# Kernel tuning notes

Hardware: AMD Instinct MI355X
Metric: run time of the kernel (lower is better)

## Reference

```python
import jax, jax.numpy as jnp
import numpy as np

N_CLASSES = 300
EMPTY = N_CLASSES
ALPHA, GAMMA = 0.25, 2.0
W_CLS, W_DOA, W_LOUD, W_CONF, W_SCE = 1.0, 1.0, 0.5, 1.0, 0.3
L_CLS, L_DOA, L_CONF = 1.0, 1.0, 0.5  # matching cost weights


def _lsa(cost):
    """Rectangular linear sum assignment (Jonker-Volgenant / e-maxx Hungarian).
    Returns (row_idx, col_idx) matching min(P,G) pairs, same optimum as scipy."""
    transposed = cost.shape[0] > cost.shape[1]
    C = cost.T if transposed else cost
    n, m = C.shape  # n <= m
    INF = float('inf')
    u = [0.0] * (n + 1)
    v = [0.0] * (m + 1)
    p = [0] * (m + 1)
    for i in range(1, n + 1):
        p[0] = i
        j0 = 0
        minv = [INF] * (m + 1)
        way = [0] * (m + 1)
        used = [False] * (m + 1)
        while True:
            used[j0] = True
            i0 = p[j0]
            delta = INF
            j1 = 0
            for j in range(1, m + 1):
                if not used[j]:
                    cur = C[i0 - 1, j - 1] - u[i0] - v[j]
                    if cur < minv[j]:
                        minv[j] = cur
                        way[j] = j0
                    if minv[j] < delta:
                        delta = minv[j]
                        j1 = j
            for j in range(m + 1):
                if used[j]:
                    u[p[j]] += delta
                    v[j] -= delta
                else:
                    minv[j] -= delta
            j0 = j1
            if p[j0] == 0:
                break
        while j0:
            j1 = way[j0]
            p[j0] = p[j1]
            j0 = j1
    rows, cols = [], []
    for j in range(1, m + 1):
        if p[j]:
            rows.append(p[j] - 1)
            cols.append(j - 1)
    r = np.asarray(rows, np.int64)
    c = np.asarray(cols, np.int64)
    if transposed:
        r, c = c, r
    return r, c


def _match(cl, dv, conf, gcls, gdoa, gmask):
    """Per-frame Hungarian matching (no-grad, host numpy), faithful to hungarian_match.
    Returns matched mask (B,T,S) bool, per-slot target class (B,T,S) int32 (EMPTY if unmatched),
    and gather index into gt slots (B,T,S) int32 (0 where unmatched; masked out later)."""
    B, T, S, C = cl.shape
    z = cl - cl.max(-1, keepdims=True)
    prob = np.exp(z)
    prob /= prob.sum(-1, keepdims=True)
    prob = prob[..., :N_CLASSES]
    dn = dv / np.maximum(np.linalg.norm(dv, axis=-1, keepdims=True), 1e-12)
    cp = 1.0 / (1.0 + np.exp(-conf))
    matched = np.zeros((B, T, S), bool)
    tgt = np.full((B, T, S), EMPTY, np.int32)
    gidx = np.zeros((B, T, S), np.int32)
    for b in range(B):
        for t in range(T):
            act = np.nonzero(gmask[b, t])[0]
            if act.size == 0:
                continue
            gc = gcls[b, t, act]
            gd = gdoa[b, t, act]
            gdn = gd / np.maximum(np.linalg.norm(gd, axis=-1, keepdims=True), 1e-12)
            cost = (L_CLS * (-prob[b, t][:, gc])
                    + L_DOA * (1.0 - dn[b, t] @ gdn.T)
                    + L_CONF * (1.0 - cp[b, t])[:, None])
            r, c = _lsa(cost.astype(np.float64))
            matched[b, t, r] = True
            tgt[b, t, r] = gc[c]
            gidx[b, t, r] = act[c]
    return matched, tgt, gidx


def _loss(class_logits, doa_vec, loudness, confidence, sce_vec, gt_doa, gt_loud,
          matched, tgt_cls, gidx):
    B, T, S, _ = class_logits.shape
    dt = class_logits.dtype
    mf = matched.astype(dt)                      # (B,T,S)
    # focal loss (target = matched gt class, else EMPTY)
    logp = jax.nn.log_softmax(class_logits, axis=-1)
    ce = -jnp.take_along_axis(logp, tgt_cls[..., None].astype(jnp.int32), axis=-1)[..., 0]
    f = ALPHA * (1.0 - jnp.exp(-ce)) ** GAMMA * ce
    Gm = mf.sum(-1)                              # (B,T) matched count
    Um = S - Gm
    safeG = jnp.maximum(Gm, 1.0)
    safeU = jnp.maximum(Um, 1.0)
    cls_fr = (jnp.where(Gm > 0, (f * mf).sum(-1) / safeG, 0.0)
              + jnp.where(Um > 0, (f * (1.0 - mf)).sum(-1) / safeU, 0.0))
    # gather matched gt doa / loud per slot
    g3 = jnp.broadcast_to(gidx[..., None].astype(jnp.int32), gt_doa.shape)
    mdoa = jnp.take_along_axis(gt_doa, g3, axis=2)       # (B,T,S,3)
    mloud = jnp.take_along_axis(gt_loud, gidx.astype(jnp.int32), axis=2)
    # DOA cosine distance (torch cosine_similarity eps=1e-8)
    eps = 1e-8
    num = (doa_vec * mdoa).sum(-1)
    den = (jnp.maximum(jnp.linalg.norm(doa_vec, axis=-1), eps)
           * jnp.maximum(jnp.linalg.norm(mdoa, axis=-1), eps))
    d = 1.0 - num / den
    doa_fr = jnp.where(Gm > 0, (d * mf).sum(-1) / safeG, 0.0)
    # smooth L1 (beta=1)
    diff = loudness - mloud
    ad = jnp.abs(diff)
    sl1 = jnp.where(ad < 1.0, 0.5 * diff * diff, ad - 0.5)
    loud_fr = jnp.where(Gm > 0, (sl1 * mf).sum(-1) / safeG, 0.0)
    # BCE-with-logits, target = matched indicator (zeros if no gt)
    bce = jax.nn.softplus(confidence) - confidence * mf
    conf_fr = bce.mean(-1)
    # SCE: mse(sce, gt_doa * exp(gt_loud/20)) over matched slots
    gt_sce = mdoa * jnp.exp(mloud / 20.0)[..., None]
    sq = ((sce_vec - gt_sce) ** 2).mean(-1)
    sce_fr = jnp.where(Gm > 0, (sq * mf).sum(-1) / safeG, 0.0)
    norm = float(B * T)
    cls_l = W_CLS * cls_fr.sum() / norm
    doa_l = W_DOA * doa_fr.sum() / norm
    loud_l = W_LOUD * loud_fr.sum() / norm
    conf_l = W_CONF * conf_fr.sum() / norm
    sce_l = W_SCE * sce_fr.sum() / norm
    total = cls_l + doa_l + loud_l + conf_l + sce_l
    return jnp.stack([cls_l, doa_l, loud_l, conf_l, sce_l, total])


def setup_inputs() -> dict:
    key = jax.random.key(0)
    ks = jax.random.split(key, 9)
    B, T, S = 32, 256, 8
    C = N_CLASSES + 1
    return {
        "class_logits": jax.random.normal(ks[0], (B, T, S, C), jnp.float32),
        "doa_vec": jax.random.normal(ks[1], (B, T, S, 3), jnp.float32),
        "loudness": jax.random.normal(ks[2], (B, T, S), jnp.float32),
        "confidence": jax.random.normal(ks[3], (B, T, S), jnp.float32),
        "sce_vec": jax.random.normal(ks[4], (B, T, S, 3), jnp.float32),
        "gt_cls": jax.random.randint(ks[5], (B, T, S), 0, N_CLASSES, jnp.int32),
        "gt_doa": jax.random.normal(ks[6], (B, T, S, 3), jnp.float32),
        "gt_loud": jax.random.normal(ks[7], (B, T, S), jnp.float32),
        "gt_mask": jax.random.bernoulli(ks[8], 0.5, (B, T, S)),
    }


def reference(class_logits, doa_vec, loudness, confidence, sce_vec,
              gt_cls, gt_doa, gt_loud, gt_mask):
    matched, tgt, gidx = _match(np.asarray(class_logits), np.asarray(doa_vec),
                                np.asarray(confidence), np.asarray(gt_cls),
                                np.asarray(gt_doa), np.asarray(gt_mask))
    return _loss(class_logits, doa_vec, loudness, confidence, sce_vec,
                 gt_doa, gt_loud,
                 jnp.asarray(matched), jnp.asarray(tgt), jnp.asarray(gidx))
```

## Files before the change

### kernel.cpp

```cpp
#include <hip/hip_runtime.h>
#include <math.h>

#define NFRAMES 8192
#define NS 8
#define NC 301
#define NBLOCKS (NFRAMES / 4)

#define GLOBAL_AS __attribute__((address_space(1)))
#define LDS_AS    __attribute__((address_space(3)))

__device__ float g_partial[5 * NFRAMES];

__device__ __forceinline__ float readlanef(float x, int l) {
    return __int_as_float(__builtin_amdgcn_readlane(__float_as_int(x), l));
}

#define SWZ_F(x, OFF) __int_as_float(__builtin_amdgcn_ds_swizzle(__float_as_int(x), (OFF)))
#define SWZ_I(x, OFF) __builtin_amdgcn_ds_swizzle((x), (OFF))
#define OFF_X4  0x101F
#define OFF_X16 0x401F

#define DPP_F(x, CTRL) __int_as_float(__builtin_amdgcn_update_dpp(0, __float_as_int(x), (CTRL), 0xF, 0xF, true))
#define DPP_I(x, CTRL) __builtin_amdgcn_update_dpp(0, (x), (CTRL), 0xF, 0xF, true)
#define CTRL_X1 0xB1
#define CTRL_X2 0x4E
#define CTRL_X8 0x128

__global__ __launch_bounds__(256) void frame_kernel(
    const float* __restrict__ logits,
    const float* __restrict__ doa,
    const float* __restrict__ loud,
    const float* __restrict__ conf,
    const float* __restrict__ sce,
    const int*   __restrict__ gcls,
    const float* __restrict__ gdoa,
    const float* __restrict__ gloud,
    const unsigned int* __restrict__ gmaskw)
{
    __shared__ float lgs[4][NS * NC];

    const int lane = threadIdx.x & 63;
    const int wv   = threadIdx.x >> 6;
    const int f    = blockIdx.x * 4 + wv;
    const int s    = lane >> 3;
    const int g    = lane & 7;

    {
        const float4* src = reinterpret_cast<const float4*>(logits + (size_t)f * (NS * NC));
        char* dstb = reinterpret_cast<char*>(&lgs[wv][0]);
#pragma unroll
        for (int k = 0; k < 9; k++) {
            __builtin_amdgcn_global_load_lds(
                (const GLOBAL_AS void*)(src + (k << 6) + lane),
                (LDS_AS void*)(dstb + (k << 10)), 16, 0, 0);
        }
        if (lane < 602 - 576) {
            __builtin_amdgcn_global_load_lds(
                (const GLOBAL_AS void*)(src + 576 + lane),
                (LDS_AS void*)(dstb + 9 * 1024), 16, 0, 0);
        }
    }

    unsigned int mwd = gmaskw[lane];
    unsigned long long blo = __ballot((mwd & 0xFFFFFF00u) != 0);
    unsigned long long bf1 = __ballot(mwd == 0x3f800000u);
    const int mode = (blo == 0ull) ? 0 : (bf1 ? 2 : 1);

    float L_loud = 0.f, L_cf = 0.f, L_dx = 0.f, L_dy = 0.f, L_dz = 0.f;
    float L_s0 = 0.f, L_s1 = 0.f, L_s2 = 0.f;
    if (lane < 8) {
        size_t base = (size_t)f * NS + lane;
        L_loud = loud[base];  L_cf = conf[base];
        L_dx = doa[base * 3]; L_dy = doa[base * 3 + 1]; L_dz = doa[base * 3 + 2];
        L_s0 = sce[base * 3]; L_s1 = sce[base * 3 + 1]; L_s2 = sce[base * 3 + 2];
    }
    int gcv = (lane < 8) ? gcls[f * NS + lane] : 0;

    size_t sb3 = ((size_t)f * NS + s) * 3;
    float dxr = doa[sb3], dyr = doa[sb3 + 1], dzr = doa[sb3 + 2];
    float nn = fmaxf(sqrtf(dxr * dxr + dyr * dyr + dzr * dzr), 1e-12f);
    float dnx = dxr / nn, dny = dyr / nn, dnz = dzr / nn;
    float cp = 1.f / (1.f + __expf(-conf[(size_t)f * NS + s]));

    asm volatile("s_waitcnt vmcnt(0)" ::: "memory");

    const float* ls = &lgs[wv][s * NC];

    float z0 = 0.f, z1 = 0.f, z2 = 0.f, z3 = 0.f;
#pragma unroll
    for (int k = 0; k + 3 < 37; k += 4) {
        int c0 = g + (k << 3);
        z0 += __expf(ls[c0]);
        z1 += __expf(ls[c0 + 8]);
        z2 += __expf(ls[c0 + 16]);
        z3 += __expf(ls[c0 + 24]);
    }
    z0 += __expf(ls[g + (36 << 3)]);
    {
        int c = g + (37 << 3);
        if (c < NC) z1 += __expf(ls[c]);
    }
    float z = (z0 + z1) + (z2 + z3);
    z += DPP_F(z, CTRL_X1);
    z += DPP_F(z, CTRL_X2);
    z += SWZ_F(z, OFF_X4);
    const float A = __logf(z);
    const float lossA = __shfl(A, (lane & 7) << 3);

    int slotcls = __shfl(gcv, g);
    float myLgat = lgs[wv][s * NC + slotcls];
    float lossL300 = (lane < 8) ? lgs[wv][lane * NC + 300] : 0.f;

    bool on = false;
    if (lane < 8) {
        int idx = f * NS + lane;
        if (mode == 0)      on = ((const int*)gmaskw)[idx] != 0;
        else if (mode == 1) on = ((const unsigned char*)gmaskw)[idx] != 0;
        else                on = ((const float*)gmaskw)[idx] != 0.f;
    }
    unsigned long long bal = __ballot(on);
    const unsigned int actmask = (unsigned int)(bal & 0xFFull);
    const int G = __popc(actmask);

    int act_reg = 0;
    float gdx = 0.f, gdy = 0.f, gdz = 0.f;
    float rgx = 0.f, rgy = 0.f, rgz = 0.f, rgl = 0.f;
    if (lane < G) {
        unsigned int mk = actmask;
        for (int t = 0; t < lane; t++) mk &= mk - 1;
        int slot = __ffs(mk) - 1;
        act_reg = slot;
        size_t b3 = (size_t)(f * NS + slot) * 3;
        float x = gdoa[b3], y = gdoa[b3 + 1], zz = gdoa[b3 + 2];
        rgx = x; rgy = y; rgz = zz;
        rgl = gloud[(size_t)f * NS + slot];
        float n = fmaxf(sqrtf(x * x + y * y + zz * zz), 1e-12f);
        gdx = x / n; gdy = y / n; gdz = zz / n;
    }

    int   ag = __shfl(act_reg, g);
    float gx = __shfl(gdx, g), gy = __shfl(gdy, g), gz = __shfl(gdz, g);
    float lgt_c = __shfl(myLgat, (lane & 56) | ag);
    float costreg = INFINITY;
    if (g < G) {
        float pr = __expf(lgt_c - A);
        float dt = dnx * gx + dny * gy + dnz * gz;
        costreg = -pr + (1.f - dt) + 0.5f * (1.f - cp);
    }

    float d0 = (lane == 0) ? 0.f : INFINITY;
    float d1 = INFINITY, d2 = INFINITY, d3 = INFINITY;
    unsigned int par0 = 0, par1 = 0, par2 = 0, par3 = 0;

    for (int i = 0; i < G; i++) {
        float cc0 = readlanef(costreg,      i);
        float cc1 = readlanef(costreg,  8 + i);
        float cc2 = readlanef(costreg, 16 + i);
        float cc3 = readlanef(costreg, 24 + i);
        float cc4 = readlanef(costreg, 32 + i);
        float cc5 = readlanef(costreg, 40 + i);
        float cc6 = readlanef(costreg, 48 + i);
        float cc7 = readlanef(costreg, 56 + i);

        float n0, n1, n2, n3; int b0i, b1i, b2i, b3i;

#define DP_LOW6(dk, bestv, bestb)                                                    \
        {                                                                            \
            float best = INFINITY; int bb = 0; float nb, cand;                       \
            nb = DPP_F(dk, CTRL_X1); cand = (lane & 1)  ? nb + cc0 : INFINITY; if (cand < best) { best = cand; bb = 0; } \
            nb = DPP_F(dk, CTRL_X2); cand = (lane & 2)  ? nb + cc1 : INFINITY; if (cand < best) { best = cand; bb = 1; } \
            nb = SWZ_F(dk, OFF_X4);  cand = (lane & 4)  ? nb + cc2 : INFINITY; if (cand < best) { best = cand; bb = 2; } \
            nb = DPP_F(dk, CTRL_X8); cand = (lane & 8)  ? nb + cc3 : INFINITY; if (cand < best) { best = cand; bb = 3; } \
            nb = SWZ_F(dk, OFF_X16); cand = (lane & 16) ? nb + cc4 : INFINITY; if (cand < best) { best = cand; bb = 4; } \
            nb = __shfl_xor(dk, 32); cand = (lane & 32) ? nb + cc5 : INFINITY; if (cand < best) { best = cand; bb = 5; } \
            bestv = best; bestb = bb;                                                \
        }

        DP_LOW6(d0, n0, b0i)
        DP_LOW6(d1, n1, b1i)
        DP_LOW6(d2, n2, b2i)
        DP_LOW6(d3, n3, b3i)
#undef DP_LOW6
        { float cand = d0 + cc6; if (cand < n1) { n1 = cand; b1i = 6; } }
        { float cand = d2 + cc6; if (cand < n3) { n3 = cand; b3i = 6; } }
        { float cand = d0 + cc7; if (cand < n2) { n2 = cand; b2i = 7; } }
        { float cand = d1 + cc7; if (cand < n3) { n3 = cand; b3i = 7; } }

        d0 = n0; d1 = n1; d2 = n2; d3 = n3;
        int sh = 3 * i;
        par0 |= (unsigned)b0i << sh;
        par1 |= (unsigned)b1i << sh;
        par2 |= (unsigned)b2i << sh;
        par3 |= (unsigned)b3i << sh;
    }

    int mm_ = 0, mygt = 0;
    if (G > 0) {
        float vv = d0; int bm = lane;
        if (d1 < vv) { vv = d1; bm = lane | 64; }
        if (d2 < vv) { vv = d2; bm = lane | 128; }
        if (d3 < vv) { vv = d3; bm = lane | 192; }
        { float ov = DPP_F(vv, CTRL_X1); int om = DPP_I(bm, CTRL_X1); if (ov < vv || (ov == vv && om < bm)) { vv = ov; bm = om; } }
        { float ov = DPP_F(vv, CTRL_X2); int om = DPP_I(bm, CTRL_X2); if (ov < vv || (ov == vv && om < bm)) { vv = ov; bm = om; } }
        { float ov = SWZ_F(vv, OFF_X4);  int om = SWZ_I(bm, OFF_X4);  if (ov < vv || (ov == vv && om < bm)) { vv = ov; bm = om; } }
        { float ov = DPP_F(vv, CTRL_X8); int om = DPP_I(bm, CTRL_X8); if (ov < vv || (ov == vv && om < bm)) { vv = ov; bm = om; } }
        { float ov = SWZ_F(vv, OFF_X16); int om = SWZ_I(bm, OFF_X16); if (ov < vv || (ov == vv && om < bm)) { vv = ov; bm = om; } }
        { float ov = __shfl_xor(vv, 32); int om = __shfl_xor(bm, 32); if (ov < vv || (ov == vv && om < bm)) { vv = ov; bm = om; } }
        int mask = bm;
        for (int i = G - 1; i >= 0; i--) {
            int owner = mask & 63, kk = mask >> 6;
            unsigned qsel = (kk == 0) ? par0 : (kk == 1) ? par1
                          : (kk == 2) ? par2 : par3;
            unsigned qv = (unsigned)__builtin_amdgcn_readlane((int)qsel, owner);
            int p = (qv >> (3 * i)) & 7;
            if (lane == p) { mm_ = 1; mygt = i; }
            mask ^= 1 << p;
        }
    }

    int   gidx_v = __shfl(act_reg, mygt);
    float lgt_m  = __shfl(myLgat, ((lane & 7) << 3) + gidx_v);
    float mdx = __shfl(rgx, mygt), mdy = __shfl(rgy, mygt), mdz = __shfl(rgz, mygt);
    float ml  = __shfl(rgl, mygt);

    if (lane < 8) {
        int ss = lane;
        float mf = (float)mm_;
        float lgt = mm_ ? lgt_m : lossL300;
        float ce = lossA - lgt;
        float t1 = 1.f - __expf(-ce);
        float fce = 0.25f * t1 * t1 * ce;

        float num = L_dx * mdx + L_dy * mdy + L_dz * mdz;
        float den = fmaxf(sqrtf(L_dx * L_dx + L_dy * L_dy + L_dz * L_dz), 1e-8f) *
                    fmaxf(sqrtf(mdx * mdx + mdy * mdy + mdz * mdz), 1e-8f);
        float dterm = 1.f - num / den;

        float diff = L_loud - ml;
        float ad = fabsf(diff);
        float sl1 = (ad < 1.f) ? 0.5f * diff * diff : (ad - 0.5f);

        float sp = fmaxf(L_cf, 0.f) + __logf(1.f + __expf(-fabsf(L_cf)));
        float bce = sp - L_cf * mf;

        float el = __expf(ml * 0.05f);
        float e0 = L_s0 - mdx * el;
        float e1 = L_s1 - mdy * el;
        float e2 = L_s2 - mdz * el;
        float sq = (e0 * e0 + e1 * e1 + e2 * e2) * (1.f / 3.f);

        float c_m  = fce * mf;
        float c_u  = fce * (1.f - mf);
        float dsum = dterm * mf;
        float lsum = sl1 * mf;
        float qsum = sq * mf;
        float bsum = bce;
#define RED8(x) x += DPP_F(x, CTRL_X1); x += DPP_F(x, CTRL_X2); x += SWZ_F(x, OFF_X4);
        RED8(c_m) RED8(c_u) RED8(dsum) RED8(lsum) RED8(qsum) RED8(bsum)
#undef RED8
        if (ss == 0) {
            float Gm = (float)G, Um = (float)(NS - G);
            g_partial[0 * NFRAMES + f] = (G > 0 ? c_m / Gm : 0.f) + (G < NS ? c_u / Um : 0.f);
            g_partial[1 * NFRAMES + f] = (G > 0) ? dsum / Gm : 0.f;
            g_partial[2 * NFRAMES + f] = (G > 0) ? lsum / Gm : 0.f;
            g_partial[3 * NFRAMES + f] = bsum * (1.f / 8.f);
            g_partial[4 * NFRAMES + f] = (G > 0) ? qsum / Gm : 0.f;
        }
    }
}

__global__ __launch_bounds__(1024) void reduce_kernel(float* __restrict__ out) {
    __shared__ float red[16][5];
    const int tid  = threadIdx.x;
    const int lane = tid & 63;
    const int w    = tid >> 6;

    float a[5];
#pragma unroll
    for (int k = 0; k < 5; k++) {
        float lcl = 0.f;
        for (int i = tid; i < NFRAMES; i += 1024) lcl += g_partial[k * NFRAMES + i];
        lcl += DPP_F(lcl, CTRL_X1);
        lcl += DPP_F(lcl, CTRL_X2);
        lcl += SWZ_F(lcl, OFF_X4);
        lcl += DPP_F(lcl, CTRL_X8);
        lcl += SWZ_F(lcl, OFF_X16);
        lcl += __shfl_xor(lcl, 32);
        a[k] = lcl;
    }
    if (lane == 0) {
#pragma unroll
        for (int k = 0; k < 5; k++) red[w][k] = a[k];
    }
    __syncthreads();
    if (tid == 0) {
        float acc[5] = {0.f, 0.f, 0.f, 0.f, 0.f};
        for (int ww = 0; ww < 16; ww++)
#pragma unroll
            for (int k = 0; k < 5; k++) acc[k] += red[ww][k];
        const float inv_norm = 1.f / (float)NFRAMES;
        float cls_l  = 1.0f * acc[0] * inv_norm;
        float doa_l  = 1.0f * acc[1] * inv_norm;
        float loud_l = 0.5f * acc[2] * inv_norm;
        float conf_l = 1.0f * acc[3] * inv_norm;
        float sce_l  = 0.3f * acc[4] * inv_norm;
        out[0] = cls_l; out[1] = doa_l; out[2] = loud_l;
        out[3] = conf_l; out[4] = sce_l;
        out[5] = cls_l + doa_l + loud_l + conf_l + sce_l;
    }
}

extern "C" void kernel_launch(void* const* d_in, const int* in_sizes, int n_in,
                              void* d_out, int out_size, void* d_ws, size_t ws_size,
                              hipStream_t stream) {
    const float* logits = (const float*)d_in[0];
    const float* doa    = (const float*)d_in[1];
    const float* loudn  = (const float*)d_in[2];
    const float* confi  = (const float*)d_in[3];
    const float* sce    = (const float*)d_in[4];
    const int*   gcls   = (const int*)d_in[5];
    const float* gdoa   = (const float*)d_in[6];
    const float* gloud  = (const float*)d_in[7];
    const unsigned int* gmask = (const unsigned int*)d_in[8];
    float* out = (float*)d_out;

    frame_kernel<<<NBLOCKS, 256, 0, stream>>>(logits, doa, loudn, confi, sce,
                                              gcls, gdoa, gloud, gmask);
    reduce_kernel<<<1, 1024, 0, stream>>>(out);
}
```

Measured before the change: 46.31 us.

## Add predicted-slot-indexed bitmask DP fast path for frames with at most six GTs

```diff
diff --git a/kernel.cpp b/kernel.cpp
--- a/kernel.cpp
+++ b/kernel.cpp
@@ -148,54 +148,98 @@
         costreg = -pr + (1.f - dt) + 0.5f * (1.f - cp);
     }
 
-    float d0 = (lane == 0) ? 0.f : INFINITY;
-    float d1 = INFINITY, d2 = INFINITY, d3 = INFINITY;
-    unsigned int par0 = 0, par1 = 0, par2 = 0, par3 = 0;
-
-    for (int i = 0; i < G; i++) {
-        float cc0 = readlanef(costreg,      i);
-        float cc1 = readlanef(costreg,  8 + i);
-        float cc2 = readlanef(costreg, 16 + i);
-        float cc3 = readlanef(costreg, 24 + i);
-        float cc4 = readlanef(costreg, 32 + i);
-        float cc5 = readlanef(costreg, 40 + i);
-        float cc6 = readlanef(costreg, 48 + i);
-        float cc7 = readlanef(costreg, 56 + i);
-
-        float n0, n1, n2, n3; int b0i, b1i, b2i, b3i;
+    int mm_ = 0, mygt = 0;
+
+    if (G > 0 && G <= 6) {
+        float dp = (lane == 0) ? 0.f : INFINITY;
+        unsigned int par = 0;
+#pragma unroll
+        for (int i = 0; i < 8; i++) {
+            float best = dp; int pj = 15;
+            if (0 < G) { float ci = readlanef(costreg, 8 * i + 0);
+                float nb = DPP_F(dp, CTRL_X1);
+                float cand = (lane & 1)  ? nb + ci : INFINITY;
+                if (cand < best) { best = cand; pj = 0; } }
+            if (1 < G) { float ci = readlanef(costreg, 8 * i + 1);
+                float nb = DPP_F(dp, CTRL_X2);
+                float cand = (lane & 2)  ? nb + ci : INFINITY;
+                if (cand < best) { best = cand; pj = 1; } }
+            if (2 < G) { float ci = readlanef(costreg, 8 * i + 2);
+                float nb = SWZ_F(dp, OFF_X4);
+                float cand = (lane & 4)  ? nb + ci : INFINITY;
+                if (cand < best) { best = cand; pj = 2; } }
+            if (3 < G) { float ci = readlanef(costreg, 8 * i + 3);
+                float nb = DPP_F(dp, CTRL_X8);
+                float cand = (lane & 8)  ? nb + ci : INFINITY;
+                if (cand < best) { best = cand; pj = 3; } }
+            if (4 < G) { float ci = readlanef(costreg, 8 * i + 4);
+                float nb = SWZ_F(dp, OFF_X16);
+                float cand = (lane & 16) ? nb + ci : INFINITY;
+                if (cand < best) { best = cand; pj = 4; } }
+            if (5 < G) { float ci = readlanef(costreg, 8 * i + 5);
+                float nb = __shfl_xor(dp, 32);
+                float cand = (lane & 32) ? nb + ci : INFINITY;
+                if (cand < best) { best = cand; pj = 5; } }
+            dp = best;
+            par |= (unsigned)pj << (4 * i);
+        }
+        int mask = (1 << G) - 1;
+#pragma unroll
+        for (int i = 7; i >= 0; i--) {
+            unsigned pv = (unsigned)__builtin_amdgcn_readlane((int)par, mask);
+            int nib = (pv >> (4 * i)) & 15;
+            if (nib != 15) {
+                if (lane == i) { mm_ = 1; mygt = nib; }
+                mask ^= 1 << nib;
+            }
+        }
+    } else if (G > 0) {
+        float d0 = (lane == 0) ? 0.f : INFINITY;
+        float d1 = INFINITY, d2 = INFINITY, d3 = INFINITY;
+        unsigned int par0 = 0, par1 = 0, par2 = 0, par3 = 0;
+
+        for (int i = 0; i < G; i++) {
+            float cc0 = readlanef(costreg,      i);
+            float cc1 = readlanef(costreg,  8 + i);
+            float cc2 = readlanef(costreg, 16 + i);
+            float cc3 = readlanef(costreg, 24 + i);
+            float cc4 = readlanef(costreg, 32 + i);
+            float cc5 = readlanef(costreg, 40 + i);
+            float cc6 = readlanef(costreg, 48 + i);
+            float cc7 = readlanef(costreg, 56 + i);
+
+            float n0, n1, n2, n3; int b0i, b1i, b2i, b3i;
 
 #define DP_LOW6(dk, bestv, bestb)                                                    \
-        {                                                                            \
-            float best = INFINITY; int bb = 0; float nb, cand;                       \
-            nb = DPP_F(dk, CTRL_X1); cand = (lane & 1)  ? nb + cc0 : INFINITY; if (cand < best) { best = cand; bb = 0; } \
-            nb = DPP_F(dk, CTRL_X2); cand = (lane & 2)  ? nb + cc1 : INFINITY; if (cand < best) { best = cand; bb = 1; } \
-            nb = SWZ_F(dk, OFF_X4);  cand = (lane & 4)  ? nb + cc2 : INFINITY; if (cand < best) { best = cand; bb = 2; } \
-            nb = DPP_F(dk, CTRL_X8); cand = (lane & 8)  ? nb + cc3 : INFINITY; if (cand < best) { best = cand; bb = 3; } \
-            nb = SWZ_F(dk, OFF_X16); cand = (lane & 16) ? nb + cc4 : INFINITY; if (cand < best) { best = cand; bb = 4; } \
-            nb = __shfl_xor(dk, 32); cand = (lane & 32) ? nb + cc5 : INFINITY; if (cand < best) { best = cand; bb = 5; } \
-            bestv = best; bestb = bb;                                                \
-        }
-
-        DP_LOW6(d0, n0, b0i)
-        DP_LOW6(d1, n1, b1i)
-        DP_LOW6(d2, n2, b2i)
-        DP_LOW6(d3, n3, b3i)
+            {                                                                        \
+                float best = INFINITY; int bb = 0; float nb, cand;                   \
+                nb = DPP_F(dk, CTRL_X1); cand = (lane & 1)  ? nb + cc0 : INFINITY; if (cand < best) { best = cand; bb = 0; } \
+                nb = DPP_F(dk, CTRL_X2); cand = (lane & 2)  ? nb + cc1 : INFINITY; if (cand < best) { best = cand; bb = 1; } \
+                nb = SWZ_F(dk, OFF_X4);  cand = (lane & 4)  ? nb + cc2 : INFINITY; if (cand < best) { best = cand; bb = 2; } \
+                nb = DPP_F(dk, CTRL_X8); cand = (lane & 8)  ? nb + cc3 : INFINITY; if (cand < best) { best = cand; bb = 3; } \
+                nb = SWZ_F(dk, OFF_X16); cand = (lane & 16) ? nb + cc4 : INFINITY; if (cand < best) { best = cand; bb = 4; } \
+                nb = __shfl_xor(dk, 32); cand = (lane & 32) ? nb + cc5 : INFINITY; if (cand < best) { best = cand; bb = 5; } \
+                bestv = best; bestb = bb;                                            \
+            }
+
+            DP_LOW6(d0, n0, b0i)
+            DP_LOW6(d1, n1, b1i)
+            DP_LOW6(d2, n2, b2i)
+            DP_LOW6(d3, n3, b3i)
 #undef DP_LOW6
-        { float cand = d0 + cc6; if (cand < n1) { n1 = cand; b1i = 6; } }
-        { float cand = d2 + cc6; if (cand < n3) { n3 = cand; b3i = 6; } }
-        { float cand = d0 + cc7; if (cand < n2) { n2 = cand; b2i = 7; } }
-        { float cand = d1 + cc7; if (cand < n3) { n3 = cand; b3i = 7; } }
-
-        d0 = n0; d1 = n1; d2 = n2; d3 = n3;
-        int sh = 3 * i;
-        par0 |= (unsigned)b0i << sh;
-        par1 |= (unsigned)b1i << sh;
-        par2 |= (unsigned)b2i << sh;
-        par3 |= (unsigned)b3i << sh;
-    }
-
-    int mm_ = 0, mygt = 0;
-    if (G > 0) {
+            { float cand = d0 + cc6; if (cand < n1) { n1 = cand; b1i = 6; } }
+            { float cand = d2 + cc6; if (cand < n3) { n3 = cand; b3i = 6; } }
+            { float cand = d0 + cc7; if (cand < n2) { n2 = cand; b2i = 7; } }
+            { float cand = d1 + cc7; if (cand < n3) { n3 = cand; b3i = 7; } }
+
+            d0 = n0; d1 = n1; d2 = n2; d3 = n3;
+            int sh = 3 * i;
+            par0 |= (unsigned)b0i << sh;
+            par1 |= (unsigned)b1i << sh;
+            par2 |= (unsigned)b2i << sh;
+            par3 |= (unsigned)b3i << sh;
+        }
+
         float vv = d0; int bm = lane;
         if (d1 < vv) { vv = d1; bm = lane | 64; }
         if (d2 < vv) { vv = d2; bm = lane | 128; }
```

New measurement: 43.15 us. 1.07x faster.
